# Optimization experiments

Measured on AMD Instinct MI355X. Metric: run time of the kernel, lower is better.

## Reference

```python
import jax, jax.numpy as jnp
import numpy as np

N, Z_DIM = 131072, 64
K_CODES = 2048
QUANT_TEMP = 0.0  # default T when 'quant_temp' not passed


def setup_inputs() -> dict:
    key = jax.random.key(0)
    k1, k2 = jax.random.split(key)
    z = jax.random.normal(k1, (N, Z_DIM), dtype=jnp.float32)
    e = jax.random.normal(k2, (K_CODES, Z_DIM), dtype=jnp.float32)
    return {"z": z, "e": e}


def reference(z, e):
    # torch.cdist -> euclidean distance matrix [N, K]; argmin over squared
    # distance gives identical indices (sqrt is monotone), so skip the sqrt.
    # ||z - e||^2 = ||z||^2 - 2 z.e^T + ||e||^2
    z_sq = jnp.sum(z * z, axis=1, keepdims=True)          # [N, 1]
    e_sq = jnp.sum(e * e, axis=1)                          # [K]
    d2 = z_sq - 2.0 * (z @ e.T) + e_sq[None, :]            # [N, K]
    min_indices = jnp.argmin(d2, axis=1)                   # [N] int
    z_q = e[min_indices]                                   # gather [N, Z]
    commit_loss = jnp.mean((z - z_q) ** 2)                 # F.mse_loss
    # straight-through: z + (1 - T) * stop_grad(z_q - z), T = 0
    z_out = z + (1.0 - QUANT_TEMP) * jax.lax.stop_gradient(z_q - z)
    return z_out, min_indices, commit_loss
```

## Files before the change

kernel.cpp:

```cpp
#include <hip/hip_runtime.h>


#define N_ROWS 131072
#define ZD 64
#define KCODES 2048
#define RF 4
#define EPS_S 2e-3f
#define FLAG_CAP 32768

using bf16x8  = __attribute__((ext_vector_type(8))) short;
using floatx4 = __attribute__((ext_vector_type(4))) float;

__device__ inline float bf2f(unsigned short u) {
    union { unsigned int i; float f; } c; c.i = ((unsigned int)u) << 16; return c.f;
}
__device__ inline unsigned short f2bf(float x) {
    union { float f; unsigned int i; } c; c.f = x;
    unsigned int b = c.i + 0x7FFFu + ((c.i >> 16) & 1u);
    return (unsigned short)(b >> 16);
}


__global__ void prep_kernel(const float* __restrict__ e, float* __restrict__ ws) {
    int t = threadIdx.x, lane = t & 63, w = t >> 6;
    if (blockIdx.x == 0 && t == 0) { ws[0] = 0.0f; ((unsigned int*)ws)[1] = 0u; }
    int c = blockIdx.x * 4 + w;
    float* esn = ws + 1024;
    double* esq64 = (double*)((char*)ws + 16384);
    unsigned short* et = (unsigned short*)((char*)ws + 32768);
    float* eT = (float*)((char*)ws + 557056);

    float x = e[(size_t)c * ZD + lane];
    unsigned short h = f2bf(x);
    unsigned short l = f2bf(x - bf2f(h));
    size_t base = ((size_t)(c >> 4) << 11) + ((lane >> 3) << 7) + ((c & 15) << 3) + (lane & 7);
    et[base]        = h;
    et[base + 1024] = l;
    eT[lane * KCODES + c] = x;
    double s = (double)x * (double)x;
    for (int off = 1; off < 64; off <<= 1) s += __shfl_xor(s, off, 64);
    if (lane == 0) { esq64[c] = s; esn[c] = (float)(-0.5 * s); }
}

#define MFMA_T(H0, H1, L0, L1, EN, NACC, NACC2) do {                         \
    floatx4 _ai = {EN, EN, EN, EN};                                          \
    floatx4 _zi = {0.0f, 0.0f, 0.0f, 0.0f};                                  \
    _Pragma("unroll")                                                        \
    for (int _rf = 0; _rf < RF; _rf++) {                                     \
        floatx4 a1 = _ai;                                                    \
        floatx4 a2 = _zi;                                                    \
        a1 = __builtin_amdgcn_mfma_f32_16x16x32_bf16(Ah[_rf][0], H0, a1, 0, 0, 0); \
        a2 = __builtin_amdgcn_mfma_f32_16x16x32_bf16(Ah[_rf][1], H1, a2, 0, 0, 0); \
        a1 = __builtin_amdgcn_mfma_f32_16x16x32_bf16(Ah[_rf][0], L0, a1, 0, 0, 0); \
        a2 = __builtin_amdgcn_mfma_f32_16x16x32_bf16(Ah[_rf][1], L1, a2, 0, 0, 0); \
        a1 = __builtin_amdgcn_mfma_f32_16x16x32_bf16(Al[_rf][0], H0, a1, 0, 0, 0); \
        a2 = __builtin_amdgcn_mfma_f32_16x16x32_bf16(Al[_rf][1], H1, a2, 0, 0, 0); \
        NACC[_rf] = a1; NACC2[_rf] = a2;                                     \
    }                                                                        \
} while (0)

#define ARGMAX_T(PACC, PACC2, FPREV) do {                                    \
    _Pragma("unroll")                                                        \
    for (int _rf = 0; _rf < RF; _rf++) {                                     \
        _Pragma("unroll")                                                    \
        for (int _r = 0; _r < 4; _r++) {                                     \
            float _s  = PACC[_rf][_r] + PACC2[_rf][_r];                      \
            bool  _gt = _s > mval[_rf][_r];                                  \
            mv2[_rf][_r]  = __builtin_amdgcn_fmed3f(_s, mval[_rf][_r], mv2[_rf][_r]); \
            midx[_rf][_r] = _gt ? (FPREV) : midx[_rf][_r];                   \
            mval[_rf][_r] = fmaxf(_s, mval[_rf][_r]);                        \
        }                                                                    \
    }                                                                        \
} while (0)

#define STAGE(BUF, TILE) do {                                                \
    const char* _src = etiles + ((size_t)((TILE) & 127) << 12)               \
                       + ((size_t)threadIdx.x << 4);                         \
    __builtin_amdgcn_global_load_lds(                                        \
        (const __attribute__((address_space(1))) unsigned int*)_src,         \
        (__attribute__((address_space(3))) unsigned int*)&tilebuf[BUF][w << 10], \
        16, 0, 0);                                                           \
} while (0)

#define READT(BUF, H0, H1, L0, L1) do {                                      \
    H0 = *(const bf16x8*)(const void*)(tilebuf[BUF] + (lane << 4));          \
    H1 = *(const bf16x8*)(const void*)(tilebuf[BUF] + 1024 + (lane << 4));   \
    L0 = *(const bf16x8*)(const void*)(tilebuf[BUF] + 2048 + (lane << 4));   \
    L1 = *(const bf16x8*)(const void*)(tilebuf[BUF] + 3072 + (lane << 4));   \
} while (0)

#define ITER_P(BUF, CT, NACC, NACC2, PACC, PACC2) do {                       \
    STAGE((BUF) ^ 1, (CT) + 1);                                              \
    float _en = esn_sm[(CT) * 16 + lrow];                                    \
    bf16x8 h0, h1, l0, l1;                                                   \
    READT(BUF, h0, h1, l0, l1);                                              \
    MFMA_T(h0, h1, l0, l1, _en, NACC, NACC2);                                \
    ARGMAX_T(PACC, PACC2, fprev);                                            \
    fprev += 16.0f;                                                          \
    __syncthreads();                                                         \
} while (0)

__global__ __launch_bounds__(256, 2) void vq_mfma(
        const float* __restrict__ z, const float* __restrict__ e,
        float* __restrict__ ws, float* __restrict__ out) {
    const char* etiles = (const char*)ws + 32768;
    unsigned int* cntp  = (unsigned int*)ws + 1;
    unsigned int* flags = (unsigned int*)((char*)ws + 1081344);

    __shared__ __attribute__((aligned(16))) char tilebuf[2][4096];
    __shared__ __attribute__((aligned(16))) float esn_sm[KCODES];

    int lane = threadIdx.x & 63;
    int w    = threadIdx.x >> 6;
    int wid  = blockIdx.x * 4 + w;
    int row0 = wid * (RF * 16);
    int lrow = lane & 15;
    int lq   = lane >> 4;

    {
        const char* esrc = (const char*)ws + 4096 + ((size_t)threadIdx.x << 4);
        __builtin_amdgcn_global_load_lds(
            (const __attribute__((address_space(1))) unsigned int*)esrc,
            (__attribute__((address_space(3))) unsigned int*)((char*)esn_sm + (w << 10)),
            16, 0, 0);
        __builtin_amdgcn_global_load_lds(
            (const __attribute__((address_space(1))) unsigned int*)(esrc + 4096),
            (__attribute__((address_space(3))) unsigned int*)((char*)esn_sm + 4096 + (w << 10)),
            16, 0, 0);
    }
    STAGE(0, 0);

    bf16x8 Ah[RF][2], Al[RF][2];
#pragma unroll
    for (int rf = 0; rf < RF; rf++)
#pragma unroll
        for (int kc = 0; kc < 2; kc++) {
            const float* zp = z + (size_t)(row0 + rf * 16 + lrow) * ZD + kc * 32 + lq * 8;
            float xv[8];
            *(float4*)(void*)&xv[0] = *(const float4*)(const void*)zp;
            *(float4*)(void*)&xv[4] = *(const float4*)(const void*)(zp + 4);
            bf16x8 h, l;
#pragma unroll
            for (int j = 0; j < 8; j++) {
                unsigned short hb = f2bf(xv[j]);
                h[j] = (short)hb;
                l[j] = (short)f2bf(xv[j] - bf2f(hb));
            }
            Ah[rf][kc] = h; Al[rf][kc] = l;
            asm volatile("" : "+v"(Ah[rf][kc]), "+v"(Al[rf][kc]));
        }

    floatx4 mval[RF], mv2[RF], midx[RF];
#pragma unroll
    for (int rf = 0; rf < RF; rf++)
#pragma unroll
        for (int r = 0; r < 4; r++) {
            mval[rf][r] = -3.0e38f; mv2[rf][r] = -3.0e38f; midx[rf][r] = 0.0f;
        }

    floatx4 aA[RF], aA2[RF], aB[RF], aB2[RF];
    float fprev = (float)lrow;
    __syncthreads();

    {
        STAGE(1, 1);
        float _en = esn_sm[lrow];
        bf16x8 h0, h1, l0, l1;
        READT(0, h0, h1, l0, l1);
        MFMA_T(h0, h1, l0, l1, _en, aA, aA2);
        __syncthreads();
    }

    for (int ct = 1; ct < 127; ct += 2) {
        ITER_P(1, ct,     aB, aB2, aA, aA2);
        ITER_P(0, ct + 1, aA, aA2, aB, aB2);
    }

    {
        float _en = esn_sm[127 * 16 + lrow];
        bf16x8 h0, h1, l0, l1;
        READT(1, h0, h1, l0, l1);
        MFMA_T(h0, h1, l0, l1, _en, aB, aB2);
        ARGMAX_T(aA, aA2, fprev);
        fprev += 16.0f;
    }
    ARGMAX_T(aB, aB2, fprev);

    float lacc = 0.0f;
#pragma unroll
    for (int rf = 0; rf < RF; rf++)
#pragma unroll
        for (int r = 0; r < 4; r++) {
            float v = mval[rf][r], v2 = mv2[rf][r], fi = midx[rf][r];
            for (int off = 1; off < 16; off <<= 1) {
                float ov  = __shfl_xor(v,  off, 64);
                float ofi = __shfl_xor(fi, off, 64);
                float ov2 = __shfl_xor(v2, off, 64);
                bool take = (ov > v) || ((ov == v) && (ofi < fi));
                float loser = take ? v : ov;
                v2 = fmaxf(fmaxf(v2, ov2), loser);
                v  = take ? ov  : v;
                fi = take ? ofi : fi;
            }
            int row = row0 + rf * 16 + lq * 4 + r;
            int idx = (int)fi;
            float4 ev = ((const float4*)(const void*)(e + (size_t)idx * ZD))[lrow];
            float4 zv = ((const float4*)(const void*)(z + (size_t)row * ZD))[lrow];
            ((float4*)(void*)(out + (size_t)row * ZD))[lrow] = ev;
            float dx = ev.x - zv.x, dy = ev.y - zv.y;
            float dz = ev.z - zv.z, dw = ev.w - zv.w;
            lacc = fmaf(dx, dx, lacc); lacc = fmaf(dy, dy, lacc);
            lacc = fmaf(dz, dz, lacc); lacc = fmaf(dw, dw, lacc);
            if (lrow == 0) {
                out[(size_t)N_ROWS * ZD + row] = fi;
                if (v - v2 < EPS_S) {
                    unsigned int i = atomicAdd(cntp, 1u);
                    if (i < FLAG_CAP) flags[i] = (unsigned int)row;
                }
            }
        }

    for (int off = 1; off < 64; off <<= 1) lacc += __shfl_xor(lacc, off, 64);
    __shared__ float sm[4];
    if (lane == 0) sm[w] = lacc;
    __syncthreads();
    if (threadIdx.x == 0) atomicAdd(ws, sm[0] + sm[1] + sm[2] + sm[3]);
}

__global__ __launch_bounds__(256) void vq_fixup(
        const float* __restrict__ z, const float* __restrict__ e,
        float* __restrict__ ws, float* __restrict__ out) {
    const double* esq64 = (const double*)((const char*)ws + 16384);
    const float* eT = (const float*)((const char*)ws + 557056);
    const unsigned int* flags = (const unsigned int*)((const char*)ws + 1081344);
    unsigned int cnt = ((const unsigned int*)ws)[1];
    if (cnt > FLAG_CAP) cnt = FLAG_CAP;

    if (blockIdx.x == 0 && threadIdx.x == 0)
        out[(size_t)N_ROWS * ZD + N_ROWS] = ws[0] * (1.0f / 8388608.0f);

    __shared__ float zrow[ZD];
    __shared__ double sd[4]; __shared__ int si[4]; __shared__ int sbest;
    int t = threadIdx.x, lane = t & 63, w = t >> 6;

    for (unsigned int u = blockIdx.x; u < cnt; u += gridDim.x) {
        int row = (int)flags[u];
        __syncthreads();
        if (t < ZD) zrow[t] = z[(size_t)row * ZD + t];
        __syncthreads();

        double dacc[8];
#pragma unroll
        for (int j = 0; j < 8; j++) dacc[j] = 0.0;
        for (int k = 0; k < ZD; k++) {
            double zk = (double)zrow[k];
            const float* ek = eT + k * KCODES + t;
#pragma unroll
            for (int j = 0; j < 8; j++)
                dacc[j] = fma(zk, (double)ek[256 * j], dacc[j]);
        }
        double dmin = 1.0e300; int imin = 0;
#pragma unroll
        for (int j = 0; j < 8; j++) {
            int c = t + 256 * j;
            double d = fma(-2.0, dacc[j], esq64[c]);
            if (d < dmin) { dmin = d; imin = c; }
        }
        for (int off = 1; off < 64; off <<= 1) {
            double od = __shfl_xor(dmin, off, 64);
            int    oi = __shfl_xor(imin, off, 64);
            if (od < dmin || (od == dmin && oi < imin)) { dmin = od; imin = oi; }
        }
        if (lane == 0) { sd[w] = dmin; si[w] = imin; }
        __syncthreads();
        if (t == 0) {
            double bd = sd[0]; int bi = si[0];
            for (int q = 1; q < 4; q++)
                if (sd[q] < bd || (sd[q] == bd && si[q] < bi)) { bd = sd[q]; bi = si[q]; }
            sbest = bi;
        }
        __syncthreads();
        int bi = sbest;
        if (t < 16)
            ((float4*)(void*)(out + (size_t)row * ZD))[t] =
                ((const float4*)(const void*)(e + (size_t)bi * ZD))[t];
        if (t == 0) out[(size_t)N_ROWS * ZD + row] = (float)bi;
    }
}

extern "C" void kernel_launch(void* const* d_in, const int* in_sizes, int n_in,
                              void* d_out, int out_size, void* d_ws, size_t ws_size,
                              hipStream_t stream) {
    const float* z = (const float*)d_in[0];
    const float* e = (const float*)d_in[1];
    float* out = (float*)d_out;
    float* ws  = (float*)d_ws;

    prep_kernel<<<dim3(512), dim3(256), 0, stream>>>(e, ws);
    vq_mfma<<<dim3(512), dim3(256), 0, stream>>>(z, e, ws, out);
    vq_fixup<<<dim3(256), dim3(256), 0, stream>>>(z, e, ws, out);
}
```

Baseline: 201.7 us.

## Switch codebook tile staging to a 4-deep LDS ring with vmcnt-gated barriers

```diff
diff --git a/kernel.cpp b/kernel.cpp
--- a/kernel.cpp
+++ b/kernel.cpp
@@ -42,9 +42,11 @@
     if (lane == 0) { esq64[c] = s; esn[c] = (float)(-0.5 * s); }
 }
 
-#define MFMA_T(H0, H1, L0, L1, EN, NACC, NACC2) do {                         \
+#define COMPUTE(H0, H1, L0, L1, EN, FCOL) do {                               \
     floatx4 _ai = {EN, EN, EN, EN};                                          \
     floatx4 _zi = {0.0f, 0.0f, 0.0f, 0.0f};                                  \
+    floatx4 _p1[RF], _p2[RF];                                                \
+    __builtin_amdgcn_s_setprio(1);                                           \
     _Pragma("unroll")                                                        \
     for (int _rf = 0; _rf < RF; _rf++) {                                     \
         floatx4 a1 = _ai;                                                    \
@@ -55,19 +57,17 @@
         a2 = __builtin_amdgcn_mfma_f32_16x16x32_bf16(Ah[_rf][1], L1, a2, 0, 0, 0); \
         a1 = __builtin_amdgcn_mfma_f32_16x16x32_bf16(Al[_rf][0], H0, a1, 0, 0, 0); \
         a2 = __builtin_amdgcn_mfma_f32_16x16x32_bf16(Al[_rf][1], H1, a2, 0, 0, 0); \
-        NACC[_rf] = a1; NACC2[_rf] = a2;                                     \
+        _p1[_rf] = a1; _p2[_rf] = a2;                                        \
     }                                                                        \
-} while (0)
-
-#define ARGMAX_T(PACC, PACC2, FPREV) do {                                    \
+    __builtin_amdgcn_s_setprio(0);                                           \
     _Pragma("unroll")                                                        \
     for (int _rf = 0; _rf < RF; _rf++) {                                     \
         _Pragma("unroll")                                                    \
         for (int _r = 0; _r < 4; _r++) {                                     \
-            float _s  = PACC[_rf][_r] + PACC2[_rf][_r];                      \
+            float _s  = _p1[_rf][_r] + _p2[_rf][_r];                         \
             bool  _gt = _s > mval[_rf][_r];                                  \
             mv2[_rf][_r]  = __builtin_amdgcn_fmed3f(_s, mval[_rf][_r], mv2[_rf][_r]); \
-            midx[_rf][_r] = _gt ? (FPREV) : midx[_rf][_r];                   \
+            midx[_rf][_r] = _gt ? (FCOL) : midx[_rf][_r];                    \
             mval[_rf][_r] = fmaxf(_s, mval[_rf][_r]);                        \
         }                                                                    \
     }                                                                        \
@@ -89,15 +89,15 @@
     L1 = *(const bf16x8*)(const void*)(tilebuf[BUF] + 3072 + (lane << 4));   \
 } while (0)
 
-#define ITER_P(BUF, CT, NACC, NACC2, PACC, PACC2) do {                       \
-    STAGE((BUF) ^ 1, (CT) + 1);                                              \
+#define ITER_V(CT) do {                                                      \
+    STAGE(((CT) + 2) & 3, (CT) + 2);                                         \
+    asm volatile("s_waitcnt vmcnt(2)" ::: "memory");                         \
+    __builtin_amdgcn_s_barrier();                                            \
     float _en = esn_sm[(CT) * 16 + lrow];                                    \
     bf16x8 h0, h1, l0, l1;                                                   \
-    READT(BUF, h0, h1, l0, l1);                                              \
-    MFMA_T(h0, h1, l0, l1, _en, NACC, NACC2);                                \
-    ARGMAX_T(PACC, PACC2, fprev);                                            \
-    fprev += 16.0f;                                                          \
-    __syncthreads();                                                         \
+    READT((CT) & 3, h0, h1, l0, l1);                                         \
+    COMPUTE(h0, h1, l0, l1, _en, fcol);                                      \
+    fcol += 16.0f;                                                           \
 } while (0)
 
 __global__ __launch_bounds__(256, 2) void vq_mfma(
@@ -107,7 +107,7 @@
     unsigned int* cntp  = (unsigned int*)ws + 1;
     unsigned int* flags = (unsigned int*)((char*)ws + 1081344);
 
-    __shared__ __attribute__((aligned(16))) char tilebuf[2][4096];
+    __shared__ __attribute__((aligned(16))) char tilebuf[4][4096];
     __shared__ __attribute__((aligned(16))) float esn_sm[KCODES];
 
     int lane = threadIdx.x & 63;
@@ -116,6 +116,26 @@
     int row0 = wid * (RF * 16);
     int lrow = lane & 15;
     int lq   = lane >> 4;
+
+    bf16x8 Ah[RF][2], Al[RF][2];
+#pragma unroll
+    for (int rf = 0; rf < RF; rf++)
+#pragma unroll
+        for (int kc = 0; kc < 2; kc++) {
+            const float* zp = z + (size_t)(row0 + rf * 16 + lrow) * ZD + kc * 32 + lq * 8;
+            float xv[8];
+            *(float4*)(void*)&xv[0] = *(const float4*)(const void*)zp;
+            *(float4*)(void*)&xv[4] = *(const float4*)(const void*)(zp + 4);
+            bf16x8 h, l;
+#pragma unroll
+            for (int j = 0; j < 8; j++) {
+                unsigned short hb = f2bf(xv[j]);
+                h[j] = (short)hb;
+                l[j] = (short)f2bf(xv[j] - bf2f(hb));
+            }
+            Ah[rf][kc] = h; Al[rf][kc] = l;
+            asm volatile("" : "+v"(Ah[rf][kc]), "+v"(Al[rf][kc]));
+        }
 
     {
         const char* esrc = (const char*)ws + 4096 + ((size_t)threadIdx.x << 4);
@@ -129,26 +149,7 @@
             16, 0, 0);
     }
     STAGE(0, 0);
-
-    bf16x8 Ah[RF][2], Al[RF][2];
-#pragma unroll
-    for (int rf = 0; rf < RF; rf++)
-#pragma unroll
-        for (int kc = 0; kc < 2; kc++) {
-            const float* zp = z + (size_t)(row0 + rf * 16 + lrow) * ZD + kc * 32 + lq * 8;
-            float xv[8];
-            *(float4*)(void*)&xv[0] = *(const float4*)(const void*)zp;
-            *(float4*)(void*)&xv[4] = *(const float4*)(const void*)(zp + 4);
-            bf16x8 h, l;
-#pragma unroll
-            for (int j = 0; j < 8; j++) {
-                unsigned short hb = f2bf(xv[j]);
-                h[j] = (short)hb;
-                l[j] = (short)f2bf(xv[j] - bf2f(hb));
-            }
-            Ah[rf][kc] = h; Al[rf][kc] = l;
-            asm volatile("" : "+v"(Ah[rf][kc]), "+v"(Al[rf][kc]));
-        }
+    STAGE(1, 1);
 
     floatx4 mval[RF], mv2[RF], midx[RF];
 #pragma unroll
@@ -158,33 +159,14 @@
             mval[rf][r] = -3.0e38f; mv2[rf][r] = -3.0e38f; midx[rf][r] = 0.0f;
         }
 
-    floatx4 aA[RF], aA2[RF], aB[RF], aB2[RF];
-    float fprev = (float)lrow;
-    __syncthreads();
-
-    {
-        STAGE(1, 1);
-        float _en = esn_sm[lrow];
-        bf16x8 h0, h1, l0, l1;
-        READT(0, h0, h1, l0, l1);
-        MFMA_T(h0, h1, l0, l1, _en, aA, aA2);
-        __syncthreads();
+    float fcol = (float)lrow;
+
+    for (int ct = 0; ct < 128; ct += 4) {
+        ITER_V(ct);
+        ITER_V(ct + 1);
+        ITER_V(ct + 2);
+        ITER_V(ct + 3);
     }
-
-    for (int ct = 1; ct < 127; ct += 2) {
-        ITER_P(1, ct,     aB, aB2, aA, aA2);
-        ITER_P(0, ct + 1, aA, aA2, aB, aB2);
-    }
-
-    {
-        float _en = esn_sm[127 * 16 + lrow];
-        bf16x8 h0, h1, l0, l1;
-        READT(1, h0, h1, l0, l1);
-        MFMA_T(h0, h1, l0, l1, _en, aB, aB2);
-        ARGMAX_T(aA, aA2, fprev);
-        fprev += 16.0f;
-    }
-    ARGMAX_T(aB, aB2, fprev);
 
     float lacc = 0.0f;
 #pragma unroll
```

Result: slower. 218.9 us (+8.5%).
